# Optimization experiments

Hardware: AMD Instinct MI355X
Metric: run time of the kernel (lower is better)

## Reference

```python
import jax, jax.numpy as jnp
import numpy as np

NUM_ITER = 5
DIM = 512
BATCH = 64


def setup_inputs() -> dict:
    key = jax.random.key(0)
    a = jax.random.normal(key, (BATCH, DIM, DIM), dtype=jnp.float32)
    # Symmetric PSD input (covariance-like), as in bilinear pooling; Newton-Schulz
    # requires SPD matrices for convergence.
    x = jnp.einsum('bik,bjk->bij', a, a) / DIM
    I = jnp.eye(DIM, dtype=jnp.float32)
    return {"x": x, "I": I}


def reference(x, I):
    # x: [bs, dim, dim]; I: [dim, dim]
    normA = jnp.sqrt(jnp.sum(x * x, axis=(1, 2), keepdims=True))  # Frobenius norm per matrix
    Y = x / normA
    bs, dim, _ = x.shape
    Z = jnp.broadcast_to(I, (bs, dim, dim))
    Ib = Z
    for _ in range(NUM_ITER):
        T = 0.5 * (3.0 * Ib - jnp.matmul(Z, Y))
        Y = jnp.matmul(Y, T)
        Z = jnp.matmul(T, Z)
    sA = Y * jnp.sqrt(normA)
    return sA
```

## Files before the change

### kernel.cpp

```cpp
#include <hip/hip_runtime.h>
#include <hip/hip_bf16.h>
#include <stdint.h>

#define DIM   512
#define BATCH 64
#define KENC  1024
#define BM    256
#define BN    256
#define BKT   32
#define NKT   16
#define BUFE  32768

typedef __attribute__((ext_vector_type(8))) short short8;
typedef __attribute__((ext_vector_type(4))) float floatx4;

__device__ __forceinline__ ushort f2bf(float f) {
    __hip_bfloat16 h = __float2bfloat16(f);
    return *(ushort*)&h;
}
__device__ __forceinline__ float bf2f(ushort u) {
    __hip_bfloat16 h = *(__hip_bfloat16*)&u;
    return (float)h;
}

typedef __attribute__((address_space(3))) uint32_t lds_u32;
typedef const __attribute__((address_space(1))) uint32_t glb_u32;
__device__ __forceinline__ void gload16(const ushort* g, ushort* l) {
    __builtin_amdgcn_global_load_lds((glb_u32*)g, (lds_u32*)l, 16, 0, 0);
}

#define WAITVM(N) asm volatile("s_waitcnt vmcnt(" #N ")" ::: "memory")
#define BARRIER() do { __builtin_amdgcn_s_barrier(); __builtin_amdgcn_sched_barrier(0); } while (0)

__global__ __launch_bounds__(256) void norm_partial_kernel(const float* __restrict__ x,
                                                           float* __restrict__ partial) {
    int b = blockIdx.y;
    int i = blockIdx.x;
    const float4* xv = (const float4*)(x + (size_t)b * DIM * DIM + (size_t)i * (DIM * DIM / 16));
    float s = 0.f;
    #pragma unroll
    for (int r = 0; r < 16; ++r) {
        float4 v = xv[r * 256 + threadIdx.x];
        s += v.x * v.x + v.y * v.y + v.z * v.z + v.w * v.w;
    }
    #pragma unroll
    for (int off = 32; off > 0; off >>= 1) s += __shfl_down(s, off, 64);
    __shared__ float red[4];
    int lane = threadIdx.x & 63, wid = threadIdx.x >> 6;
    if (lane == 0) red[wid] = s;
    __syncthreads();
    if (threadIdx.x == 0) partial[b * 16 + i] = red[0] + red[1] + red[2] + red[3];
}

__global__ __launch_bounds__(256) void init_kernel(const float* __restrict__ x,
                                                   const float* __restrict__ partial,
                                                   float* __restrict__ norms,
                                                   ushort* __restrict__ Yenc,
                                                   ushort* __restrict__ Tenc) {
    int b = blockIdx.y;
    float s = 0.f;
    #pragma unroll
    for (int p = 0; p < 16; ++p) s += partial[b * 16 + p];
    float nrm = sqrtf(s);
    if (blockIdx.x == 0 && threadIdx.x == 0) norms[b] = nrm;
    float inv = 1.0f / nrm;
    int idx = (blockIdx.x * 256 + threadIdx.x) * 4;
    int r = idx >> 9;
    int c = idx & 511;
    float4 v = *(const float4*)(x + (size_t)b * DIM * DIM + idx);
    float yv[4] = {v.x * inv, v.y * inv, v.z * inv, v.w * inv};
    size_t base = (size_t)b * DIM * KENC + (size_t)r * KENC;
    ushort yhi[4], ylo[4], thi[4], tlo[4];
    #pragma unroll
    for (int j = 0; j < 4; ++j) {
        float y = yv[j];
        yhi[j] = f2bf(y);
        ylo[j] = f2bf(y - bf2f(yhi[j]));
        float t = ((c + j) == r ? 1.5f : 0.0f) - 0.5f * y;
        thi[j] = f2bf(t);
        tlo[j] = f2bf(t - bf2f(thi[j]));
    }
    *(ushort4*)(Yenc + base + c)       = *(ushort4*)yhi;
    *(ushort4*)(Yenc + base + 512 + c) = *(ushort4*)ylo;
    *(ushort4*)(Tenc + base + c)       = *(ushort4*)thi;
    *(ushort4*)(Tenc + base + 512 + c) = *(ushort4*)tlo;
}

__device__ __forceinline__ void stage_hi(ushort* buf, const ushort* Ag, const ushort* Bg,
                                         int k0, int tid) {
    #pragma unroll
    for (int s = 0; s < 2; ++s) {
        int vt = tid + s * 512;
        int row = vt >> 2;
        int pc  = vt & 3;
        int kc  = ((pc ^ ((row >> 1) & 3)) << 3);
        const ushort* ar = Ag + (size_t)row * KENC + k0 + kc;
        const ushort* br = Bg + (size_t)row * KENC + k0 + kc;
        gload16(ar, &buf[vt * 8]);
        gload16(br, &buf[16384 + vt * 8]);
    }
}
__device__ __forceinline__ void stage_lo(ushort* buf, const ushort* Ag, const ushort* Bg,
                                         int k0, int tid) {
    #pragma unroll
    for (int s = 0; s < 2; ++s) {
        int vt = tid + s * 512;
        int row = vt >> 2;
        int pc  = vt & 3;
        int kc  = ((pc ^ ((row >> 1) & 3)) << 3);
        const ushort* ar = Ag + (size_t)row * KENC + k0 + kc;
        const ushort* br = Bg + (size_t)row * KENC + k0 + kc;
        gload16(ar + 512, &buf[8192 + vt * 8]);
        gload16(br + 512, &buf[24576 + vt * 8]);
    }
}

__device__ __forceinline__ void store_enc(ushort* Cenc, size_t matoff, int gr, int gc, float v) {
    ushort hi = f2bf(v);
    ushort lo = f2bf(v - bf2f(hi));
    Cenc[matoff + (size_t)gr * KENC + gc] = hi;
    Cenc[matoff + (size_t)gr * KENC + 512 + gc] = lo;
}

template <int MODE>
__global__ __launch_bounds__(512, 2) void gemm_bt(const ushort* __restrict__ A,
                                                  const ushort* __restrict__ B,
                                                  ushort* __restrict__ Cenc,
                                                  float* __restrict__ Cout,
                                                  const float* __restrict__ norms) {
    __shared__ __attribute__((aligned(16))) ushort sm[2 * BUFE];

    int f = blockIdx.x;
    int xcd = f & 7;
    int g   = f >> 3;
    int b   = xcd + 8 * (g >> 2);
    int t   = g & 3;
    int bm  = t >> 1;
    int bn  = t & 1;

    size_t matoff = (size_t)b * DIM * KENC;
    const ushort* Ag = A + matoff + (size_t)bm * BM * KENC;
    const ushort* Bg = B + matoff + (size_t)bn * BN * KENC;

    int tid = threadIdx.x;
    int wave = tid >> 6, lane = tid & 63;
    int lane15 = lane & 15, quad = lane >> 4;
    int wrow = (wave >> 2) * 128;
    int wcol = (wave & 3) * 64;
    int s2 = (lane15 >> 1) & 3;
    int fo = ((quad ^ s2) << 3);

    floatx4 acc[8][4];
    #pragma unroll
    for (int i = 0; i < 8; ++i)
        #pragma unroll
        for (int j = 0; j < 4; ++j)
            acc[i][j] = (floatx4){0.f, 0.f, 0.f, 0.f};

    stage_hi(sm, Ag, Bg, 0, tid);
    stage_lo(sm, Ag, Bg, 0, tid);
    WAITVM(4);
    BARRIER();

    #pragma unroll 2
    for (int kt = 0; kt < NKT; ++kt) {
        const ushort* cur = sm + (kt & 1) * BUFE;
        ushort* nxt = sm + ((kt + 1) & 1) * BUFE;
        const ushort* Ash = cur;
        const ushort* Asl = cur + 8192;
        const ushort* Bsh = cur + 16384;
        const ushort* Bsl = cur + 24576;

        short8 ab[8], bb[4], xl[4];

        #pragma unroll
        for (int i = 0; i < 8; ++i)
            ab[i] = *(const short8*)&Ash[(wrow + i * 16 + lane15) * BKT + fo];
        #pragma unroll
        for (int j = 0; j < 4; ++j)
            bb[j] = *(const short8*)&Bsh[(wcol + j * 16 + lane15) * BKT + fo];
        if (kt + 1 < NKT) {
            stage_hi(nxt, Ag, Bg, (kt + 1) * BKT, tid);
            WAITVM(4);
        } else {
            WAITVM(0);
        }
        BARRIER();
        __builtin_amdgcn_s_setprio(1);
        #pragma unroll
        for (int i = 0; i < 8; ++i)
            #pragma unroll
            for (int j = 0; j < 4; ++j)
                acc[i][j] = __builtin_amdgcn_mfma_f32_16x16x32_bf16(ab[i], bb[j], acc[i][j], 0, 0, 0);
        __builtin_amdgcn_s_setprio(0);
        BARRIER();

        #pragma unroll
        for (int j = 0; j < 4; ++j)
            xl[j] = *(const short8*)&Bsl[(wcol + j * 16 + lane15) * BKT + fo];
        if (kt + 1 < NKT)
            stage_lo(nxt, Ag, Bg, (kt + 1) * BKT, tid);
        BARRIER();
        __builtin_amdgcn_s_setprio(1);
        #pragma unroll
        for (int i = 0; i < 8; ++i)
            #pragma unroll
            for (int j = 0; j < 4; ++j)
                acc[i][j] = __builtin_amdgcn_mfma_f32_16x16x32_bf16(ab[i], xl[j], acc[i][j], 0, 0, 0);
        __builtin_amdgcn_s_setprio(0);
        BARRIER();

        #pragma unroll
        for (int i = 0; i < 8; ++i)
            ab[i] = *(const short8*)&Asl[(wrow + i * 16 + lane15) * BKT + fo];
        BARRIER();
        __builtin_amdgcn_s_setprio(1);
        #pragma unroll
        for (int i = 0; i < 8; ++i)
            #pragma unroll
            for (int j = 0; j < 4; ++j)
                acc[i][j] = __builtin_amdgcn_mfma_f32_16x16x32_bf16(ab[i], bb[j], acc[i][j], 0, 0, 0);
        __builtin_amdgcn_s_setprio(0);
        if (kt + 1 < NKT) WAITVM(4);
        BARRIER();
    }

    float scale = (MODE == 2) ? sqrtf(norms[b]) : 0.f;
    #pragma unroll
    for (int i = 0; i < 8; ++i) {
        int gr0 = bm * BM + wrow + i * 16 + quad * 4;
        #pragma unroll
        for (int j = 0; j < 4; ++j) {
            int gc = bn * BN + wcol + j * 16 + lane15;
            #pragma unroll
            for (int rr = 0; rr < 4; ++rr) {
                int gr = gr0 + rr;
                float cv = acc[i][j][rr];
                if (MODE == 0) {
                    store_enc(Cenc, matoff, gr, gc, (gr == gc ? 1.5f : 0.0f) - 0.5f * cv);
                } else if (MODE == 1) {
                    store_enc(Cenc, matoff, gr, gc, cv);
                } else {
                    Cout[(size_t)b * DIM * DIM + (size_t)gr * DIM + gc] = cv * scale;
                }
            }
        }
    }
}

extern "C" void kernel_launch(void* const* d_in, const int* in_sizes, int n_in,
                              void* d_out, int out_size, void* d_ws, size_t ws_size,
                              hipStream_t stream) {
    const float* x = (const float*)d_in[0];
    float* out = (float*)d_out;

    const size_t MATB = (size_t)BATCH * DIM * KENC * sizeof(ushort);
    char* ws = (char*)d_ws;
    ushort* W0 = (ushort*)(ws + 0 * MATB);
    ushort* W1 = (ushort*)(ws + 1 * MATB);
    ushort* W2 = (ushort*)(ws + 2 * MATB);
    float* partial = (float*)(ws + 3 * MATB);
    float* norms   = (float*)(ws + 3 * MATB + 4096);
    ushort* D = (ushort*)d_out;

    dim3 gblk(512);
    dim3 g1(256);

    norm_partial_kernel<<<dim3(16, BATCH), 256, 0, stream>>>(x, partial);
    init_kernel<<<dim3(256, BATCH), 256, 0, stream>>>(x, partial, norms, W0, W1);

    gemm_bt<1><<<g1, gblk, 0, stream>>>(W0, W1, W2, nullptr, nullptr);
    gemm_bt<0><<<g1, gblk, 0, stream>>>(W1, W2, W0, nullptr, nullptr);
    gemm_bt<1><<<g1, gblk, 0, stream>>>(W2, W0, D, nullptr, nullptr);
    gemm_bt<1><<<g1, gblk, 0, stream>>>(W0, W1, W2, nullptr, nullptr);
    gemm_bt<0><<<g1, gblk, 0, stream>>>(W2, D, W0, nullptr, nullptr);
    gemm_bt<1><<<g1, gblk, 0, stream>>>(D, W0, W1, nullptr, nullptr);
    gemm_bt<1><<<g1, gblk, 0, stream>>>(W0, W2, D, nullptr, nullptr);
    gemm_bt<0><<<g1, gblk, 0, stream>>>(D, W1, W0, nullptr, nullptr);
    gemm_bt<1><<<g1, gblk, 0, stream>>>(W1, W0, W2, nullptr, nullptr);
    gemm_bt<1><<<g1, gblk, 0, stream>>>(W0, D, W1, nullptr, nullptr);
    gemm_bt<0><<<g1, gblk, 0, stream>>>(W1, W2, W0, nullptr, nullptr);
    gemm_bt<2><<<g1, gblk, 0, stream>>>(W2, W0, nullptr, out, norms);
}
```

Before: 752.4 us.

## Restructure GEMM main loop to interleave LDS reads with MFMA and cut barriers

Reworks the split-bf16 GEMM inner loop so that LDS fragment loads are split into halves and interleaved with MFMA groups, separated by scheduling barriers instead of workgroup barriers. The number of s_barrier calls per k-tile drops from about six to two, and the wait/barrier moves to the top of the loop. The aim is to hide LDS latency behind matrix-core work and reduce synchronisation stalls. It risks LDS buffer races: the A-low fragments are read after the second barrier without a further barrier while the next stage_lo writes go to the other buffer.

```diff
diff --git a/kernel.cpp b/kernel.cpp
--- a/kernel.cpp
+++ b/kernel.cpp
@@ -31,6 +31,7 @@
 
 #define WAITVM(N) asm volatile("s_waitcnt vmcnt(" #N ")" ::: "memory")
 #define BARRIER() do { __builtin_amdgcn_s_barrier(); __builtin_amdgcn_sched_barrier(0); } while (0)
+#define SCHED()   __builtin_amdgcn_sched_barrier(0)
 
 __global__ __launch_bounds__(256) void norm_partial_kernel(const float* __restrict__ x,
                                                            float* __restrict__ partial) {
@@ -159,8 +160,6 @@
 
     stage_hi(sm, Ag, Bg, 0, tid);
     stage_lo(sm, Ag, Bg, 0, tid);
-    WAITVM(4);
-    BARRIER();
 
     #pragma unroll 2
     for (int kt = 0; kt < NKT; ++kt) {
@@ -171,58 +170,88 @@
         const ushort* Bsh = cur + 16384;
         const ushort* Bsl = cur + 24576;
 
-        short8 ab[8], bb[4], xl[4];
-
-        #pragma unroll
-        for (int i = 0; i < 8; ++i)
-            ab[i] = *(const short8*)&Ash[(wrow + i * 16 + lane15) * BKT + fo];
+        short8 ah[8], bh[4], bl[4], al[4];
+
+        WAITVM(4);
+        BARRIER();
+
+        #pragma unroll
+        for (int i = 0; i < 4; ++i)
+            ah[i] = *(const short8*)&Ash[(wrow + i * 16 + lane15) * BKT + fo];
         #pragma unroll
         for (int j = 0; j < 4; ++j)
-            bb[j] = *(const short8*)&Bsh[(wcol + j * 16 + lane15) * BKT + fo];
-        if (kt + 1 < NKT) {
-            stage_hi(nxt, Ag, Bg, (kt + 1) * BKT, tid);
-            WAITVM(4);
-        } else {
-            WAITVM(0);
-        }
+            bh[j] = *(const short8*)&Bsh[(wcol + j * 16 + lane15) * BKT + fo];
+        if (kt + 1 < NKT) stage_hi(nxt, Ag, Bg, (kt + 1) * BKT, tid);
+        __builtin_amdgcn_s_setprio(1);
+        #pragma unroll
+        for (int i = 0; i < 4; ++i)
+            #pragma unroll
+            for (int j = 0; j < 4; ++j)
+                acc[i][j] = __builtin_amdgcn_mfma_f32_16x16x32_bf16(ah[i], bh[j], acc[i][j], 0, 0, 0);
+        __builtin_amdgcn_s_setprio(0);
+        SCHED();
+
+        #pragma unroll
+        for (int i = 4; i < 8; ++i)
+            ah[i] = *(const short8*)&Ash[(wrow + i * 16 + lane15) * BKT + fo];
+        __builtin_amdgcn_s_setprio(1);
+        #pragma unroll
+        for (int i = 4; i < 8; ++i)
+            #pragma unroll
+            for (int j = 0; j < 4; ++j)
+                acc[i][j] = __builtin_amdgcn_mfma_f32_16x16x32_bf16(ah[i], bh[j], acc[i][j], 0, 0, 0);
+        __builtin_amdgcn_s_setprio(0);
+        SCHED();
+
+        if (kt + 1 < NKT) { WAITVM(4); }
+        else             { WAITVM(0); }
         BARRIER();
-        __builtin_amdgcn_s_setprio(1);
-        #pragma unroll
-        for (int i = 0; i < 8; ++i)
-            #pragma unroll
-            for (int j = 0; j < 4; ++j)
-                acc[i][j] = __builtin_amdgcn_mfma_f32_16x16x32_bf16(ab[i], bb[j], acc[i][j], 0, 0, 0);
-        __builtin_amdgcn_s_setprio(0);
-        BARRIER();
 
         #pragma unroll
         for (int j = 0; j < 4; ++j)
-            xl[j] = *(const short8*)&Bsl[(wcol + j * 16 + lane15) * BKT + fo];
-        if (kt + 1 < NKT)
-            stage_lo(nxt, Ag, Bg, (kt + 1) * BKT, tid);
-        BARRIER();
-        __builtin_amdgcn_s_setprio(1);
-        #pragma unroll
-        for (int i = 0; i < 8; ++i)
-            #pragma unroll
-            for (int j = 0; j < 4; ++j)
-                acc[i][j] = __builtin_amdgcn_mfma_f32_16x16x32_bf16(ab[i], xl[j], acc[i][j], 0, 0, 0);
-        __builtin_amdgcn_s_setprio(0);
-        BARRIER();
-
-        #pragma unroll
-        for (int i = 0; i < 8; ++i)
-            ab[i] = *(const short8*)&Asl[(wrow + i * 16 + lane15) * BKT + fo];
-        BARRIER();
-        __builtin_amdgcn_s_setprio(1);
-        #pragma unroll
-        for (int i = 0; i < 8; ++i)
-            #pragma unroll
-            for (int j = 0; j < 4; ++j)
-                acc[i][j] = __builtin_amdgcn_mfma_f32_16x16x32_bf16(ab[i], bb[j], acc[i][j], 0, 0, 0);
-        __builtin_amdgcn_s_setprio(0);
-        if (kt + 1 < NKT) WAITVM(4);
-        BARRIER();
+            bl[j] = *(const short8*)&Bsl[(wcol + j * 16 + lane15) * BKT + fo];
+        if (kt + 1 < NKT) stage_lo(nxt, Ag, Bg, (kt + 1) * BKT, tid);
+        __builtin_amdgcn_s_setprio(1);
+        #pragma unroll
+        for (int i = 0; i < 4; ++i)
+            #pragma unroll
+            for (int j = 0; j < 4; ++j)
+                acc[i][j] = __builtin_amdgcn_mfma_f32_16x16x32_bf16(ah[i], bl[j], acc[i][j], 0, 0, 0);
+        __builtin_amdgcn_s_setprio(0);
+        SCHED();
+
+        __builtin_amdgcn_s_setprio(1);
+        #pragma unroll
+        for (int i = 4; i < 8; ++i)
+            #pragma unroll
+            for (int j = 0; j < 4; ++j)
+                acc[i][j] = __builtin_amdgcn_mfma_f32_16x16x32_bf16(ah[i], bl[j], acc[i][j], 0, 0, 0);
+        __builtin_amdgcn_s_setprio(0);
+        SCHED();
+
+        #pragma unroll
+        for (int i = 0; i < 4; ++i)
+            al[i] = *(const short8*)&Asl[(wrow + i * 16 + lane15) * BKT + fo];
+        __builtin_amdgcn_s_setprio(1);
+        #pragma unroll
+        for (int i = 0; i < 4; ++i)
+            #pragma unroll
+            for (int j = 0; j < 4; ++j)
+                acc[i][j] = __builtin_amdgcn_mfma_f32_16x16x32_bf16(al[i], bh[j], acc[i][j], 0, 0, 0);
+        __builtin_amdgcn_s_setprio(0);
+        SCHED();
+
+        #pragma unroll
+        for (int i = 0; i < 4; ++i)
+            al[i] = *(const short8*)&Asl[(wrow + (i + 4) * 16 + lane15) * BKT + fo];
+        __builtin_amdgcn_s_setprio(1);
+        #pragma unroll
+        for (int i = 0; i < 4; ++i)
+            #pragma unroll
+            for (int j = 0; j < 4; ++j)
+                acc[i + 4][j] = __builtin_amdgcn_mfma_f32_16x16x32_bf16(al[i], bh[j], acc[i + 4][j], 0, 0, 0);
+        __builtin_amdgcn_s_setprio(0);
+        SCHED();
     }
 
     float scale = (MODE == 2) ? sqrtf(norms[b]) : 0.f;
```

Result: faster. 715.8 us (-4.9%).

## Restructure GEMM main loop to prefetch hi fragments and cut barriers

Applied to the files above, without the earlier changes.

Reorganises the bf16 split-precision GEMM k-loop so the hi A/B register fragments for the next tile are loaded from LDS at the end of each iteration. The hi*hi MFMAs then overlap with the next global stage. Both lo fragments are loaded together so the hi*lo and lo*hi MFMAs run back to back. Barriers per iteration drop from about five to two. The cost is more live registers (al, bl, ah, bh all held at once), which could reduce occupancy or cause spills, and the unroll-2 pragma is removed.

```diff
diff --git a/kernel.cpp b/kernel.cpp
--- a/kernel.cpp
+++ b/kernel.cpp
@@ -162,67 +162,62 @@
     WAITVM(4);
     BARRIER();
 
-    #pragma unroll 2
+    short8 ah[8], bh[4], bl[4], al[8];
+    #pragma unroll
+    for (int i = 0; i < 8; ++i)
+        ah[i] = *(const short8*)&sm[(wrow + i * 16 + lane15) * BKT + fo];
+    #pragma unroll
+    for (int j = 0; j < 4; ++j)
+        bh[j] = *(const short8*)&sm[16384 + (wcol + j * 16 + lane15) * BKT + fo];
+
     for (int kt = 0; kt < NKT; ++kt) {
         const ushort* cur = sm + (kt & 1) * BUFE;
         ushort* nxt = sm + ((kt + 1) & 1) * BUFE;
-        const ushort* Ash = cur;
         const ushort* Asl = cur + 8192;
-        const ushort* Bsh = cur + 16384;
         const ushort* Bsl = cur + 24576;
 
-        short8 ab[8], bb[4], xl[4];
-
-        #pragma unroll
-        for (int i = 0; i < 8; ++i)
-            ab[i] = *(const short8*)&Ash[(wrow + i * 16 + lane15) * BKT + fo];
+        if (kt + 1 < NKT) stage_hi(nxt, Ag, Bg, (kt + 1) * BKT, tid);
+        __builtin_amdgcn_s_setprio(1);
+        #pragma unroll
+        for (int i = 0; i < 8; ++i)
+            #pragma unroll
+            for (int j = 0; j < 4; ++j)
+                acc[i][j] = __builtin_amdgcn_mfma_f32_16x16x32_bf16(ah[i], bh[j], acc[i][j], 0, 0, 0);
+        __builtin_amdgcn_s_setprio(0);
+
+        if (kt + 1 < NKT) { WAITVM(4); } else { WAITVM(0); }
+        BARRIER();
+
         #pragma unroll
         for (int j = 0; j < 4; ++j)
-            bb[j] = *(const short8*)&Bsh[(wcol + j * 16 + lane15) * BKT + fo];
+            bl[j] = *(const short8*)&Bsl[(wcol + j * 16 + lane15) * BKT + fo];
+        #pragma unroll
+        for (int i = 0; i < 8; ++i)
+            al[i] = *(const short8*)&Asl[(wrow + i * 16 + lane15) * BKT + fo];
+        if (kt + 1 < NKT) stage_lo(nxt, Ag, Bg, (kt + 1) * BKT, tid);
+        __builtin_amdgcn_s_setprio(1);
+        #pragma unroll
+        for (int i = 0; i < 8; ++i)
+            #pragma unroll
+            for (int j = 0; j < 4; ++j)
+                acc[i][j] = __builtin_amdgcn_mfma_f32_16x16x32_bf16(ah[i], bl[j], acc[i][j], 0, 0, 0);
+        #pragma unroll
+        for (int i = 0; i < 8; ++i)
+            #pragma unroll
+            for (int j = 0; j < 4; ++j)
+                acc[i][j] = __builtin_amdgcn_mfma_f32_16x16x32_bf16(al[i], bh[j], acc[i][j], 0, 0, 0);
+        __builtin_amdgcn_s_setprio(0);
+
         if (kt + 1 < NKT) {
-            stage_hi(nxt, Ag, Bg, (kt + 1) * BKT, tid);
             WAITVM(4);
-        } else {
-            WAITVM(0);
+            BARRIER();
+            #pragma unroll
+            for (int i = 0; i < 8; ++i)
+                ah[i] = *(const short8*)&nxt[(wrow + i * 16 + lane15) * BKT + fo];
+            #pragma unroll
+            for (int j = 0; j < 4; ++j)
+                bh[j] = *(const short8*)&nxt[16384 + (wcol + j * 16 + lane15) * BKT + fo];
         }
-        BARRIER();
-        __builtin_amdgcn_s_setprio(1);
-        #pragma unroll
-        for (int i = 0; i < 8; ++i)
-            #pragma unroll
-            for (int j = 0; j < 4; ++j)
-                acc[i][j] = __builtin_amdgcn_mfma_f32_16x16x32_bf16(ab[i], bb[j], acc[i][j], 0, 0, 0);
-        __builtin_amdgcn_s_setprio(0);
-        BARRIER();
-
-        #pragma unroll
-        for (int j = 0; j < 4; ++j)
-            xl[j] = *(const short8*)&Bsl[(wcol + j * 16 + lane15) * BKT + fo];
-        if (kt + 1 < NKT)
-            stage_lo(nxt, Ag, Bg, (kt + 1) * BKT, tid);
-        BARRIER();
-        __builtin_amdgcn_s_setprio(1);
-        #pragma unroll
-        for (int i = 0; i < 8; ++i)
-            #pragma unroll
-            for (int j = 0; j < 4; ++j)
-                acc[i][j] = __builtin_amdgcn_mfma_f32_16x16x32_bf16(ab[i], xl[j], acc[i][j], 0, 0, 0);
-        __builtin_amdgcn_s_setprio(0);
-        BARRIER();
-
-        #pragma unroll
-        for (int i = 0; i < 8; ++i)
-            ab[i] = *(const short8*)&Asl[(wrow + i * 16 + lane15) * BKT + fo];
-        BARRIER();
-        __builtin_amdgcn_s_setprio(1);
-        #pragma unroll
-        for (int i = 0; i < 8; ++i)
-            #pragma unroll
-            for (int j = 0; j < 4; ++j)
-                acc[i][j] = __builtin_amdgcn_mfma_f32_16x16x32_bf16(ab[i], bb[j], acc[i][j], 0, 0, 0);
-        __builtin_amdgcn_s_setprio(0);
-        if (kt + 1 < NKT) WAITVM(4);
-        BARRIER();
     }
 
     float scale = (MODE == 2) ? sqrtf(norms[b]) : 0.f;
```

Result: faster. 725.8 us (-3.5%).
